# Performance work log

Measured on AMD Instinct MI355X. Metric: run time of the kernel, lower is better.

## Reference

```python
import jax, jax.numpy as jnp
import numpy as np

NUM_HEADS = 32
NUM_KV_HEADS = 8
HEAD_DIM = 64
HIDDEN = 2048
EPS = 1e-05
ROPE_THETA = 1000000.0


def _rmsnorm(x, w):
    # x: [..., head_dim]
    var = jnp.mean(x * x, axis=-1, keepdims=True)
    return w * (x * jax.lax.rsqrt(var + EPS))


def _rope(q, k):
    # q,k: [B, h, T, d]
    T, d = q.shape[2], q.shape[3]
    inv_freq = 1.0 / (ROPE_THETA ** (jnp.arange(0, d, 2, dtype=jnp.float32) / d))
    t = jnp.arange(T, dtype=jnp.float32)
    freqs = jnp.outer(t, inv_freq)               # [T, d/2]
    emb = jnp.concatenate([freqs, freqs], -1)    # [T, d]
    cos = jnp.cos(emb)[None, None].astype(q.dtype)
    sin = jnp.sin(emb)[None, None].astype(q.dtype)

    def rotate(x):
        x1, x2 = x[..., : d // 2], x[..., d // 2 :]
        return jnp.concatenate([-x2, x1], -1)

    return q * cos + rotate(q) * sin, k * cos + rotate(k) * sin


def setup_inputs() -> dict:
    key = jax.random.key(0)
    ks = jax.random.split(key, 7)
    s = 0.02
    x = jax.random.normal(ks[0], (2, 2048, HIDDEN), jnp.float32)
    Wq = jax.random.normal(ks[1], (HIDDEN, NUM_HEADS * HEAD_DIM), jnp.float32) * s
    Wk = jax.random.normal(ks[2], (HIDDEN, NUM_KV_HEADS * HEAD_DIM), jnp.float32) * s
    Wv = jax.random.normal(ks[3], (HIDDEN, NUM_KV_HEADS * HEAD_DIM), jnp.float32) * s
    Wo = jax.random.normal(ks[4], (NUM_HEADS * HEAD_DIM, HIDDEN), jnp.float32) * s
    q_ln_w = jnp.ones((HEAD_DIM,), jnp.float32)
    k_ln_w = jnp.ones((HEAD_DIM,), jnp.float32)
    return {"x": x, "Wq": Wq, "Wk": Wk, "Wv": Wv, "Wo": Wo, "q_ln_w": q_ln_w, "k_ln_w": k_ln_w}


def reference(x, Wq, Wk, Wv, Wo, q_ln_w, k_ln_w):
    B, T, _ = x.shape
    g = NUM_HEADS // NUM_KV_HEADS  # GQA groups = 4
    q = (x @ Wq).reshape(B, T, NUM_HEADS, HEAD_DIM)
    k = (x @ Wk).reshape(B, T, NUM_KV_HEADS, HEAD_DIM)
    v = (x @ Wv).reshape(B, T, NUM_KV_HEADS, HEAD_DIM)
    q = _rmsnorm(q, q_ln_w)
    k = _rmsnorm(k, k_ln_w)
    q = q.transpose(0, 2, 1, 3)  # [B, nh, T, d]
    k = k.transpose(0, 2, 1, 3)  # [B, nkv, T, d]
    v = v.transpose(0, 2, 1, 3)
    q, k = _rope(q, k)
    # native GQA: fold query heads into (kv_head, group) without repeating K/V
    qg = q.reshape(B, NUM_KV_HEADS, g, T, HEAD_DIM)
    scale = 1.0 / jnp.sqrt(jnp.array(HEAD_DIM, q.dtype))
    scores = jnp.einsum("bkgtd,bksd->bkgts", qg, k) * scale  # [B,nkv,g,T,T]
    causal = jnp.tril(jnp.ones((T, T), bool))
    scores = jnp.where(causal, scores, jnp.finfo(scores.dtype).min)
    probs = jax.nn.softmax(scores, axis=-1)
    out = jnp.einsum("bkgts,bksd->bkgtd", probs, v)  # [B,nkv,g,T,d]
    out = out.reshape(B, NUM_HEADS, T, HEAD_DIM).transpose(0, 2, 1, 3).reshape(B, T, -1)
    return out @ Wo
```

## Files before the change

### kernel.cpp

```cpp
#include <hip/hip_runtime.h>
#include <cstdint>
#include <cstddef>

typedef unsigned short u16;
typedef __attribute__((ext_vector_type(8))) short short8;
typedef __attribute__((ext_vector_type(4))) short short4v;
typedef __attribute__((ext_vector_type(4))) float float4v;
typedef __attribute__((ext_vector_type(4))) unsigned short ushort4v;
typedef __attribute__((ext_vector_type(2))) float float2v;

__device__ __forceinline__ u16 f2bf(float f) {
    union { float f; uint32_t u; } x; x.f = f;
    uint32_t r = x.u + 0x7fffu + ((x.u >> 16) & 1u);
    return (u16)(r >> 16);
}
__device__ __forceinline__ uint32_t pack_bf16x2(float lo, float hi) {
    union { float f; uint32_t u; } a, b; a.f = lo; b.f = hi;
    return __builtin_amdgcn_perm(b.u + 0x8000u, a.u + 0x8000u, 0x07060302u);
}

__global__ __launch_bounds__(256) void prep(const float4v* __restrict__ x,
                                            const float* __restrict__ Wq,
                                            const float* __restrict__ Wk,
                                            const float* __restrict__ Wv,
                                            const float* __restrict__ Wo,
                                            ushort4v* __restrict__ xb,
                                            u16* __restrict__ wqkv_t,
                                            u16* __restrict__ wo_t,
                                            float2v* __restrict__ tab) {
    __shared__ float lds[32][33];
    const int bid = blockIdx.x;
    const int tid = threadIdx.x;
    if (bid < 8192) {
        const int i = bid * 256 + tid;
        float4v v = x[i];
        ushort4v o;
        #pragma unroll
        for (int j = 0; j < 4; ++j) o[j] = f2bf(v[j]);
        xb[i] = o;
        return;
    }
    if (bid < 8448) {
        const int idx = (bid - 8192) * 256 + tid;
        const int t = idx >> 5;
        const int i = idx & 31;
        const float invf = exp2f(-(float)i * (19.931568569324174f / 32.0f));
        float sv, cv;
        sincosf((float)t * invf, &sv, &cv);
        float2v o; o[0] = cv; o[1] = sv;
        tab[idx] = o;
        return;
    }
    const float* src;
    int Ns, n0, k0, scol0;
    u16* dst;
    if (bid < 14592) {
        const int id = bid - 8448;
        const int bx = id % 96, by = id / 96;
        n0 = bx * 32; k0 = by * 32;
        if (n0 < 2048)      { src = Wq; Ns = 2048; scol0 = n0; }
        else if (n0 < 2560) { src = Wk; Ns = 512;  scol0 = n0 - 2048; }
        else                { src = Wv; Ns = 512;  scol0 = n0 - 2560; }
        dst = wqkv_t;
    } else {
        const int id = bid - 14592;
        const int bx = id & 63, by = id >> 6;
        n0 = bx * 32; k0 = by * 32;
        src = Wo; Ns = 2048; scol0 = n0;
        dst = wo_t;
    }
    const int row = tid >> 3;
    const int c4  = (tid & 7) * 4;
    const float4v v = *(const float4v*)(src + (size_t)(k0 + row) * Ns + scol0 + c4);
    #pragma unroll
    for (int i = 0; i < 4; ++i) lds[row][c4 + i] = v[i];
    __syncthreads();
    const int nrow = tid >> 3;
    const int k4   = (tid & 7) * 4;
    ushort4v o;
    #pragma unroll
    for (int i = 0; i < 4; ++i) o[i] = f2bf(lds[k4 + i][nrow]);
    *(ushort4v*)(dst + (size_t)(n0 + nrow) * 2048 + k0 + k4) = o;
}

__global__ __launch_bounds__(256, 3) void gemm_bt(const u16* __restrict__ A,
                                                  const u16* __restrict__ Bt,
                                                  float* __restrict__ C,
                                                  int M, int N, int K) {
    __shared__ u16 lds_a[2][128 * 32];
    __shared__ u16 lds_b[2][128 * 32];
    const int tid  = threadIdx.x;
    const int wave = tid >> 6;
    const int lane = tid & 63;
    const int quad = lane >> 4;
    const int l15  = lane & 15;
    const long m0 = (long)blockIdx.x * 128;
    const long n0 = (long)blockIdx.y * 128;
    const int wm = (wave >> 1) * 64;
    const int wn = (wave & 1) * 64;
    const int s_row = tid >> 2;
    const int s_col = (tid & 3) * 8;

    float4v acc[4][4];
    #pragma unroll
    for (int i = 0; i < 4; ++i)
        #pragma unroll
        for (int j = 0; j < 4; ++j)
            #pragma unroll
            for (int r = 0; r < 4; ++r) acc[i][j][r] = 0.0f;

    short8 areg[2], breg[2];
    #pragma unroll
    for (int c = 0; c < 2; ++c) {
        areg[c] = *(const short8*)(A  + (m0 + c * 64 + s_row) * (long)K + s_col);
        breg[c] = *(const short8*)(Bt + (n0 + c * 64 + s_row) * (long)K + s_col);
    }
    #pragma unroll
    for (int c = 0; c < 2; ++c) {
        *(short8*)(lds_a[0] + (c * 64 + s_row) * 32 + s_col) = areg[c];
        *(short8*)(lds_b[0] + (c * 64 + s_row) * 32 + s_col) = breg[c];
    }
    __syncthreads();

    const int n_k = K >> 5;
    for (int it = 0; it < n_k; ++it) {
        const int p = it & 1;
        if (it + 1 < n_k) {
            const int kn = (it + 1) << 5;
            #pragma unroll
            for (int c = 0; c < 2; ++c) {
                areg[c] = *(const short8*)(A  + (m0 + c * 64 + s_row) * (long)K + kn + s_col);
                breg[c] = *(const short8*)(Bt + (n0 + c * 64 + s_row) * (long)K + kn + s_col);
            }
        }
        short8 af[4], bfr[4];
        #pragma unroll
        for (int mt = 0; mt < 4; ++mt)
            af[mt] = *(const short8*)(lds_a[p] + (wm + mt * 16 + l15) * 32 + quad * 8);
        #pragma unroll
        for (int nt = 0; nt < 4; ++nt)
            bfr[nt] = *(const short8*)(lds_b[p] + (wn + nt * 16 + l15) * 32 + quad * 8);
        #pragma unroll
        for (int mt = 0; mt < 4; ++mt)
            #pragma unroll
            for (int nt = 0; nt < 4; ++nt)
                acc[mt][nt] = __builtin_amdgcn_mfma_f32_16x16x32_bf16(af[mt], bfr[nt], acc[mt][nt], 0, 0, 0);
        if (it + 1 < n_k) {
            #pragma unroll
            for (int c = 0; c < 2; ++c) {
                *(short8*)(lds_a[1 - p] + (c * 64 + s_row) * 32 + s_col) = areg[c];
                *(short8*)(lds_b[1 - p] + (c * 64 + s_row) * 32 + s_col) = breg[c];
            }
        }
        __syncthreads();
    }
    #pragma unroll
    for (int mt = 0; mt < 4; ++mt) {
        #pragma unroll
        for (int nt = 0; nt < 4; ++nt) {
            const long gr = m0 + wm + mt * 16 + quad * 4;
            const long gc = n0 + wn + nt * 16 + l15;
            #pragma unroll
            for (int r = 0; r < 4; ++r)
                C[(gr + r) * N + gc] = acc[mt][nt][r];
        }
    }
}

__global__ __launch_bounds__(256, 3) void gemm_qkv(const u16* __restrict__ A,
                                                   const u16* __restrict__ Bt,
                                                   const float* __restrict__ qw,
                                                   const float* __restrict__ kw,
                                                   const float2v* __restrict__ tab,
                                                   u16* __restrict__ Qr,
                                                   u16* __restrict__ Kr,
                                                   u16* __restrict__ Vt) {
    const int K = 2048;
    __shared__ u16 lds_a[2][128 * 32];
    __shared__ u16 lds_b[2][128 * 32];
    const int tid  = threadIdx.x;
    const int wave = tid >> 6;
    const int lane = tid & 63;
    const int quad = lane >> 4;
    const int l15  = lane & 15;
    const long m0 = (long)blockIdx.x * 128;
    const long n0 = (long)blockIdx.y * 128;
    const int wm = (wave >> 1) * 64;
    const int wn = (wave & 1) * 64;
    const int s_row = tid >> 2;
    const int s_col = (tid & 3) * 8;

    float4v acc[4][4];
    #pragma unroll
    for (int i = 0; i < 4; ++i)
        #pragma unroll
        for (int j = 0; j < 4; ++j)
            #pragma unroll
            for (int r = 0; r < 4; ++r) acc[i][j][r] = 0.0f;

    short8 areg[2], breg[2];
    #pragma unroll
    for (int c = 0; c < 2; ++c) {
        areg[c] = *(const short8*)(A  + (m0 + c * 64 + s_row) * (long)K + s_col);
        breg[c] = *(const short8*)(Bt + (n0 + c * 64 + s_row) * (long)K + s_col);
    }
    #pragma unroll
    for (int c = 0; c < 2; ++c) {
        *(short8*)(lds_a[0] + (c * 64 + s_row) * 32 + s_col) = areg[c];
        *(short8*)(lds_b[0] + (c * 64 + s_row) * 32 + s_col) = breg[c];
    }
    __syncthreads();

    const int n_k = K >> 5;
    for (int it = 0; it < n_k; ++it) {
        const int p = it & 1;
        if (it + 1 < n_k) {
            const int kn = (it + 1) << 5;
            #pragma unroll
            for (int c = 0; c < 2; ++c) {
                areg[c] = *(const short8*)(A  + (m0 + c * 64 + s_row) * (long)K + kn + s_col);
                breg[c] = *(const short8*)(Bt + (n0 + c * 64 + s_row) * (long)K + kn + s_col);
            }
        }
        short8 af[4], bfr[4];
        #pragma unroll
        for (int mt = 0; mt < 4; ++mt)
            af[mt] = *(const short8*)(lds_a[p] + (wm + mt * 16 + l15) * 32 + quad * 8);
        #pragma unroll
        for (int nt = 0; nt < 4; ++nt)
            bfr[nt] = *(const short8*)(lds_b[p] + (wn + nt * 16 + l15) * 32 + quad * 8);
        #pragma unroll
        for (int mt = 0; mt < 4; ++mt)
            #pragma unroll
            for (int nt = 0; nt < 4; ++nt)
                acc[mt][nt] = __builtin_amdgcn_mfma_f32_16x16x32_bf16(af[mt], bfr[nt], acc[mt][nt], 0, 0, 0);
        if (it + 1 < n_k) {
            #pragma unroll
            for (int c = 0; c < 2; ++c) {
                *(short8*)(lds_a[1 - p] + (c * 64 + s_row) * 32 + s_col) = areg[c];
                *(short8*)(lds_b[1 - p] + (c * 64 + s_row) * 32 + s_col) = breg[c];
            }
        }
        __syncthreads();
    }

    const int col0 = (int)n0 + wn;
    if (col0 < 2560) {
        const bool isQ = (col0 < 2048);
        const float* lw = isQ ? qw : kw;
        float wreg[4];
        #pragma unroll
        for (int nt = 0; nt < 4; ++nt) wreg[nt] = lw[nt * 16 + l15];
        const float qs = isQ ? 0.18033688011112042f : 1.0f;
        u16* dst = isQ ? (Qr + ((size_t)(col0 >> 6)) * 2048 * 64)
                       : (Kr + ((size_t)((col0 - 2048) >> 6)) * 2048 * 64);
        const size_t head_stride = isQ ? ((size_t)32 * 2048 * 64) : ((size_t)8 * 2048 * 64);
        #pragma unroll
        for (int mt = 0; mt < 4; ++mt) {
            const int gr0 = (int)m0 + wm + mt * 16 + quad * 4;
            const int b = gr0 >> 11, tt0 = gr0 & 2047;
            float rms[4];
            #pragma unroll
            for (int r = 0; r < 4; ++r) {
                float s = 0.0f;
                #pragma unroll
                for (int nt = 0; nt < 4; ++nt) s += acc[mt][nt][r] * acc[mt][nt][r];
                s += __shfl_xor(s, 1);
                s += __shfl_xor(s, 2);
                s += __shfl_xor(s, 4);
                s += __shfl_xor(s, 8);
                rms[r] = rsqrtf(s * (1.0f / 64.0f) + 1e-5f);
            }
            u16* rowp = dst + (size_t)b * head_stride + (size_t)tt0 * 64;
            #pragma unroll
            for (int nt = 0; nt < 2; ++nt) {
                const int i = nt * 16 + l15;
                #pragma unroll
                for (int r = 0; r < 4; ++r) {
                    const float2v cs = tab[(tt0 + r) * 32 + i];
                    const float v1 = acc[mt][nt][r]     * rms[r] * wreg[nt];
                    const float v2 = acc[mt][nt + 2][r] * rms[r] * wreg[nt + 2];
                    const float o1 = (v1 * cs[0] - v2 * cs[1]) * qs;
                    const float o2 = (v2 * cs[0] + v1 * cs[1]) * qs;
                    rowp[(size_t)r * 64 + i]      = f2bf(o1);
                    rowp[(size_t)r * 64 + i + 32] = f2bf(o2);
                }
            }
        }
    } else {
        const int kh = (col0 - 2560) >> 6;
        #pragma unroll
        for (int mt = 0; mt < 4; ++mt) {
            const int gr0 = (int)m0 + wm + mt * 16 + quad * 4;
            const int b = gr0 >> 11, tt0 = gr0 & 2047;
            #pragma unroll
            for (int nt = 0; nt < 4; ++nt) {
                const int d = nt * 16 + l15;
                ushort4v o;
                #pragma unroll
                for (int r = 0; r < 4; ++r) o[r] = f2bf(acc[mt][nt][r]);
                *(ushort4v*)(Vt + (((size_t)(b * 8 + kh)) * 64 + d) * 2048 + tt0) = o;
            }
        }
    }
}

#define KSTR 72
#define VSTR 136
__global__ __launch_bounds__(512, 4) void attn_fwd(const u16* __restrict__ Qr,
                                                   const u16* __restrict__ Kr,
                                                   const u16* __restrict__ Vt,
                                                   u16* __restrict__ Ob) {
    __shared__ u16 lds_k[2][128 * KSTR];
    __shared__ u16 lds_vt[2][64 * VSTR];
    const int tid  = threadIdx.x;
    const int wave = tid >> 6;
    const int lane = tid & 63;
    const int quad = lane >> 4;
    const int l15  = lane & 15;
    const int qxB = blockIdx.x;
    const int qxA = 15 - qxB;
    const int bh = blockIdx.y;
    const int b = bh >> 5, h = bh & 31;
    const int kh = h >> 2;
    const u16* Qh = Qr + ((size_t)(b * 32 + h))  * 2048 * 64;
    const u16* Kh = Kr + ((size_t)(b * 8 + kh))  * 2048 * 64;
    const u16* Vh = Vt + ((size_t)(b * 8 + kh))  * 64 * 2048;

    const int k_key0 = tid >> 3;
    const int k_d0   = (tid & 7) * 8;
    const int v_d0   = tid >> 4;
    const int v_k8   = (tid & 15) * 8;

    const int qrowA = qxA * 128 + wave * 16 + l15;
    const int qrowB = qxB * 128 + wave * 16 + l15;
    short8 qfA[2], qfB[2];
    #pragma unroll
    for (int ks = 0; ks < 2; ++ks) {
        qfA[ks] = *(const short8*)(Qh + (size_t)qrowA * 64 + ks * 32 + quad * 8);
        qfB[ks] = *(const short8*)(Qh + (size_t)qrowB * 64 + ks * 32 + quad * 8);
    }
    short8 qf0 = qfA[0], qf1 = qfA[1];
    int qrow_cur = qrowA;

    float m_i = -3e38f, l_i = 0.0f;
    float4v Oacc[4];
    #pragma unroll
    for (int dt = 0; dt < 4; ++dt)
        #pragma unroll
        for (int r = 0; r < 4; ++r) Oacc[dt][r] = 0.0f;

    short8 kreg[2], vreg[2];
    #pragma unroll
    for (int i = 0; i < 2; ++i) {
        kreg[i] = *(const short8*)(Kh + (size_t)(k_key0 + i * 64) * 64 + k_d0);
        vreg[i] = *(const short8*)(Vh + (size_t)(v_d0 + i * 32) * 2048 + v_k8);
    }
    #pragma unroll
    for (int i = 0; i < 2; ++i) {
        *(short8*)(lds_k[0]  + (k_key0 + i * 64) * KSTR + k_d0) = kreg[i];
        *(short8*)(lds_vt[0] + (v_d0 + i * 32) * VSTR + v_k8)   = vreg[i];
    }
    __syncthreads();

    const int n_it = 17;
    for (int i = 0; i < n_it; ++i) {
        const int p = i & 1;
        const bool last = (i == n_it - 1);
        const int kt_cur = (i <= qxA) ? i : (i - qxA - 1);
        const int kt0 = kt_cur << 7;

        if (!last) {
            const int ip1 = i + 1;
            const int ktn = (ip1 <= qxA) ? ip1 : (ip1 - qxA - 1);
            const size_t nk0 = (size_t)(ktn << 7);
            #pragma unroll
            for (int j = 0; j < 2; ++j) {
                kreg[j] = *(const short8*)(Kh + (nk0 + k_key0 + j * 64) * 64 + k_d0);
                vreg[j] = *(const short8*)(Vh + (size_t)(v_d0 + j * 32) * 2048 + nk0 + v_k8);
            }
        }

        float4v S[8];
        #pragma unroll
        for (int nt = 0; nt < 8; ++nt)
            #pragma unroll
            for (int r = 0; r < 4; ++r) S[nt][r] = 0.0f;
        #pragma unroll
        for (int ks = 0; ks < 2; ++ks) {
            const short8 qf = ks ? qf1 : qf0;
            #pragma unroll
            for (int nt = 0; nt < 8; ++nt) {
                short8 kf = *(const short8*)(lds_k[p] + (nt * 16 + l15) * KSTR + ks * 32 + quad * 8);
                S[nt] = __builtin_amdgcn_mfma_f32_16x16x32_bf16(kf, qf, S[nt], 0, 0, 0);
            }
        }
        if (i == qxA || last) {
            #pragma unroll
            for (int nt = 0; nt < 8; ++nt) {
                const int keyb = kt0 + nt * 16 + quad * 4;
                #pragma unroll
                for (int r = 0; r < 4; ++r)
                    if (keyb + r > qrow_cur) S[nt][r] = -3e38f;
            }
        }
        float mx = S[0][0];
        #pragma unroll
        for (int nt = 0; nt < 8; ++nt)
            #pragma unroll
            for (int r = 0; r < 4; ++r) mx = fmaxf(mx, S[nt][r]);
        mx = fmaxf(mx, __shfl_xor(mx, 16));
        mx = fmaxf(mx, __shfl_xor(mx, 32));
        const float mnew = fmaxf(m_i, mx);
        const float alpha = __builtin_amdgcn_exp2f(m_i - mnew);
        m_i = mnew;
        float rs = 0.0f;
        #pragma unroll
        for (int nt = 0; nt < 8; ++nt)
            #pragma unroll
            for (int r = 0; r < 4; ++r) {
                const float pv = __builtin_amdgcn_exp2f(S[nt][r] - mnew);
                S[nt][r] = pv;
                rs += pv;
            }
        rs += __shfl_xor(rs, 16);
        rs += __shfl_xor(rs, 32);
        l_i = l_i * alpha + rs;
        #pragma unroll
        for (int dt = 0; dt < 4; ++dt)
            #pragma unroll
            for (int r = 0; r < 4; ++r) Oacc[dt][r] *= alpha;

        #pragma unroll
        for (int nt = 0; nt < 8; ++nt) {
            union { uint32_t u[2]; short4v s; } pu;
            pu.u[0] = pack_bf16x2(S[nt][0], S[nt][1]);
            pu.u[1] = pack_bf16x2(S[nt][2], S[nt][3]);
            const short4v pf = pu.s;
            #pragma unroll
            for (int dt = 0; dt < 4; ++dt) {
                const short4v vf = *(const short4v*)(lds_vt[p] + (dt * 16 + l15) * VSTR + nt * 16 + quad * 4);
                Oacc[dt] = __builtin_amdgcn_mfma_f32_16x16x16bf16_1k(vf, pf, Oacc[dt], 0, 0, 0);
            }
        }

        if (i == qxA) {
            const float rl = 1.0f / l_i;
            #pragma unroll
            for (int dt = 0; dt < 4; ++dt) {
                ushort4v o;
                #pragma unroll
                for (int r = 0; r < 4; ++r) o[r] = f2bf(Oacc[dt][r] * rl);
                *(ushort4v*)(Ob + ((size_t)(b * 2048 + qrowA)) * 2048 + h * 64 + dt * 16 + quad * 4) = o;
            }
            m_i = -3e38f;
            l_i = 0.0f;
            qf0 = qfB[0];
            qf1 = qfB[1];
            qrow_cur = qrowB;
        }

        if (!last) {
            #pragma unroll
            for (int j = 0; j < 2; ++j) {
                *(short8*)(lds_k[1 - p]  + (k_key0 + j * 64) * KSTR + k_d0) = kreg[j];
                *(short8*)(lds_vt[1 - p] + (v_d0 + j * 32) * VSTR + v_k8)   = vreg[j];
            }
        }
        __syncthreads();
    }
    const float rl = 1.0f / l_i;
    #pragma unroll
    for (int dt = 0; dt < 4; ++dt) {
        ushort4v o;
        #pragma unroll
        for (int r = 0; r < 4; ++r) o[r] = f2bf(Oacc[dt][r] * rl);
        *(ushort4v*)(Ob + ((size_t)(b * 2048 + qrowB)) * 2048 + h * 64 + dt * 16 + quad * 4) = o;
    }
}

extern "C" void kernel_launch(void* const* d_in, const int* in_sizes, int n_in,
                              void* d_out, int out_size, void* d_ws, size_t ws_size,
                              hipStream_t stream) {
    (void)in_sizes; (void)n_in; (void)out_size; (void)ws_size;
    const float* x  = (const float*)d_in[0];
    const float* Wq = (const float*)d_in[1];
    const float* Wk = (const float*)d_in[2];
    const float* Wv = (const float*)d_in[3];
    const float* Wo = (const float*)d_in[4];
    const float* qw = (const float*)d_in[5];
    const float* kw = (const float*)d_in[6];
    float* out = (float*)d_out;

    char* ws = (char*)d_ws;
    size_t off = 0;
    auto alloc = [&](size_t bytes) {
        char* p = ws + off;
        off += (bytes + 255) & ~(size_t)255;
        return p;
    };
    u16* xb     = (u16*)alloc((size_t)8388608 * 2);
    u16* wqkv_t = (u16*)alloc((size_t)3072 * 2048 * 2);
    u16* wo_t   = (u16*)alloc((size_t)2048 * 2048 * 2);
    u16* q_r    = (u16*)alloc((size_t)2 * 32 * 2048 * 64 * 2);
    u16* k_r    = (u16*)alloc((size_t)2 * 8 * 2048 * 64 * 2);
    u16* v_r    = (u16*)alloc((size_t)2 * 8 * 64 * 2048 * 2);
    float2v* rtab = (float2v*)alloc((size_t)2048 * 32 * 8);
    u16* attnb  = xb;

    hipLaunchKernelGGL(prep, dim3(18688), dim3(256), 0, stream,
                       (const float4v*)x, Wq, Wk, Wv, Wo,
                       (ushort4v*)xb, wqkv_t, wo_t, rtab);
    hipLaunchKernelGGL(gemm_qkv, dim3(32, 24), dim3(256), 0, stream,
                       xb, wqkv_t, qw, kw, rtab, q_r, k_r, v_r);
    hipLaunchKernelGGL(attn_fwd, dim3(8, 64), dim3(512), 0, stream, q_r, k_r, v_r, attnb);
    hipLaunchKernelGGL(gemm_bt, dim3(32, 16), dim3(256), 0, stream,
                       attnb, wo_t, out, 4096, 2048, 2048);
}
```

Before: 295.5 us.

## Use direct global-to-LDS loads in GEMMs and lazy softmax rescaling in attention

The two GEMM kernels drop the register-staged double-buffered LDS pipeline and instead load tiles straight from global memory into a single LDS buffer using global_load_lds, with a barrier before and after the compute. This removes the VGPR staging and ds_write instructions and halves LDS use, but it no longer overlaps the next tile's global loads with the current MFMAs. In attention, the online-softmax rescale of O and l is skipped unless the row max grows by more than 8 (in log2 units), which saves exp and multiply work per tile. Because that path now skips the alpha multiply, Oacc is explicitly zeroed when a query row finishes.

```diff
diff --git a/kernel.cpp b/kernel.cpp
--- a/kernel.cpp
+++ b/kernel.cpp
@@ -17,6 +17,11 @@
 __device__ __forceinline__ uint32_t pack_bf16x2(float lo, float hi) {
     union { float f; uint32_t u; } a, b; a.f = lo; b.f = hi;
     return __builtin_amdgcn_perm(b.u + 0x8000u, a.u + 0x8000u, 0x07060302u);
+}
+__device__ __forceinline__ void gl_lds16(const u16* g, u16* l) {
+    __builtin_amdgcn_global_load_lds(
+        (const __attribute__((address_space(1))) void*)g,
+        (__attribute__((address_space(3))) void*)l, 16, 0, 0);
 }
 
 __global__ __launch_bounds__(256) void prep(const float4v* __restrict__ x,
@@ -87,8 +92,8 @@
                                                   const u16* __restrict__ Bt,
                                                   float* __restrict__ C,
                                                   int M, int N, int K) {
-    __shared__ u16 lds_a[2][128 * 32];
-    __shared__ u16 lds_b[2][128 * 32];
+    __shared__ u16 lds_a[128 * 32];
+    __shared__ u16 lds_b[128 * 32];
     const int tid  = threadIdx.x;
     const int wave = tid >> 6;
     const int lane = tid & 63;
@@ -109,49 +114,33 @@
             #pragma unroll
             for (int r = 0; r < 4; ++r) acc[i][j][r] = 0.0f;
 
-    short8 areg[2], breg[2];
-    #pragma unroll
-    for (int c = 0; c < 2; ++c) {
-        areg[c] = *(const short8*)(A  + (m0 + c * 64 + s_row) * (long)K + s_col);
-        breg[c] = *(const short8*)(Bt + (n0 + c * 64 + s_row) * (long)K + s_col);
-    }
-    #pragma unroll
-    for (int c = 0; c < 2; ++c) {
-        *(short8*)(lds_a[0] + (c * 64 + s_row) * 32 + s_col) = areg[c];
-        *(short8*)(lds_b[0] + (c * 64 + s_row) * 32 + s_col) = breg[c];
-    }
-    __syncthreads();
+    const u16* ga0 = A  + (m0 + s_row) * (long)K + s_col;
+    const u16* ga1 = ga0 + 64 * (long)K;
+    const u16* gb0 = Bt + (n0 + s_row) * (long)K + s_col;
+    const u16* gb1 = gb0 + 64 * (long)K;
+    u16* la = lds_a + tid * 8;
+    u16* lb = lds_b + tid * 8;
 
     const int n_k = K >> 5;
     for (int it = 0; it < n_k; ++it) {
-        const int p = it & 1;
-        if (it + 1 < n_k) {
-            const int kn = (it + 1) << 5;
-            #pragma unroll
-            for (int c = 0; c < 2; ++c) {
-                areg[c] = *(const short8*)(A  + (m0 + c * 64 + s_row) * (long)K + kn + s_col);
-                breg[c] = *(const short8*)(Bt + (n0 + c * 64 + s_row) * (long)K + kn + s_col);
-            }
-        }
+        const int k0 = it << 5;
+        gl_lds16(ga0 + k0, la);
+        gl_lds16(ga1 + k0, la + 2048);
+        gl_lds16(gb0 + k0, lb);
+        gl_lds16(gb1 + k0, lb + 2048);
+        __syncthreads();
         short8 af[4], bfr[4];
         #pragma unroll
         for (int mt = 0; mt < 4; ++mt)
-            af[mt] = *(const short8*)(lds_a[p] + (wm + mt * 16 + l15) * 32 + quad * 8);
+            af[mt] = *(const short8*)(lds_a + (wm + mt * 16 + l15) * 32 + quad * 8);
         #pragma unroll
         for (int nt = 0; nt < 4; ++nt)
-            bfr[nt] = *(const short8*)(lds_b[p] + (wn + nt * 16 + l15) * 32 + quad * 8);
+            bfr[nt] = *(const short8*)(lds_b + (wn + nt * 16 + l15) * 32 + quad * 8);
         #pragma unroll
         for (int mt = 0; mt < 4; ++mt)
             #pragma unroll
             for (int nt = 0; nt < 4; ++nt)
                 acc[mt][nt] = __builtin_amdgcn_mfma_f32_16x16x32_bf16(af[mt], bfr[nt], acc[mt][nt], 0, 0, 0);
-        if (it + 1 < n_k) {
-            #pragma unroll
-            for (int c = 0; c < 2; ++c) {
-                *(short8*)(lds_a[1 - p] + (c * 64 + s_row) * 32 + s_col) = areg[c];
-                *(short8*)(lds_b[1 - p] + (c * 64 + s_row) * 32 + s_col) = breg[c];
-            }
-        }
         __syncthreads();
     }
     #pragma unroll
@@ -176,8 +165,8 @@
                                                    u16* __restrict__ Kr,
                                                    u16* __restrict__ Vt) {
     const int K = 2048;
-    __shared__ u16 lds_a[2][128 * 32];
-    __shared__ u16 lds_b[2][128 * 32];
+    __shared__ u16 lds_a[128 * 32];
+    __shared__ u16 lds_b[128 * 32];
     const int tid  = threadIdx.x;
     const int wave = tid >> 6;
     const int lane = tid & 63;
@@ -198,49 +187,33 @@
             #pragma unroll
             for (int r = 0; r < 4; ++r) acc[i][j][r] = 0.0f;
 
-    short8 areg[2], breg[2];
-    #pragma unroll
-    for (int c = 0; c < 2; ++c) {
-        areg[c] = *(const short8*)(A  + (m0 + c * 64 + s_row) * (long)K + s_col);
-        breg[c] = *(const short8*)(Bt + (n0 + c * 64 + s_row) * (long)K + s_col);
-    }
-    #pragma unroll
-    for (int c = 0; c < 2; ++c) {
-        *(short8*)(lds_a[0] + (c * 64 + s_row) * 32 + s_col) = areg[c];
-        *(short8*)(lds_b[0] + (c * 64 + s_row) * 32 + s_col) = breg[c];
-    }
-    __syncthreads();
+    const u16* ga0 = A  + (m0 + s_row) * (long)K + s_col;
+    const u16* ga1 = ga0 + 64 * (long)K;
+    const u16* gb0 = Bt + (n0 + s_row) * (long)K + s_col;
+    const u16* gb1 = gb0 + 64 * (long)K;
+    u16* la = lds_a + tid * 8;
+    u16* lb = lds_b + tid * 8;
 
     const int n_k = K >> 5;
     for (int it = 0; it < n_k; ++it) {
-        const int p = it & 1;
-        if (it + 1 < n_k) {
-            const int kn = (it + 1) << 5;
-            #pragma unroll
-            for (int c = 0; c < 2; ++c) {
-                areg[c] = *(const short8*)(A  + (m0 + c * 64 + s_row) * (long)K + kn + s_col);
-                breg[c] = *(const short8*)(Bt + (n0 + c * 64 + s_row) * (long)K + kn + s_col);
-            }
-        }
+        const int k0 = it << 5;
+        gl_lds16(ga0 + k0, la);
+        gl_lds16(ga1 + k0, la + 2048);
+        gl_lds16(gb0 + k0, lb);
+        gl_lds16(gb1 + k0, lb + 2048);
+        __syncthreads();
         short8 af[4], bfr[4];
         #pragma unroll
         for (int mt = 0; mt < 4; ++mt)
-            af[mt] = *(const short8*)(lds_a[p] + (wm + mt * 16 + l15) * 32 + quad * 8);
+            af[mt] = *(const short8*)(lds_a + (wm + mt * 16 + l15) * 32 + quad * 8);
         #pragma unroll
         for (int nt = 0; nt < 4; ++nt)
-            bfr[nt] = *(const short8*)(lds_b[p] + (wn + nt * 16 + l15) * 32 + quad * 8);
+            bfr[nt] = *(const short8*)(lds_b + (wn + nt * 16 + l15) * 32 + quad * 8);
         #pragma unroll
         for (int mt = 0; mt < 4; ++mt)
             #pragma unroll
             for (int nt = 0; nt < 4; ++nt)
                 acc[mt][nt] = __builtin_amdgcn_mfma_f32_16x16x32_bf16(af[mt], bfr[nt], acc[mt][nt], 0, 0, 0);
-        if (it + 1 < n_k) {
-            #pragma unroll
-            for (int c = 0; c < 2; ++c) {
-                *(short8*)(lds_a[1 - p] + (c * 64 + s_row) * 32 + s_col) = areg[c];
-                *(short8*)(lds_b[1 - p] + (c * 64 + s_row) * 32 + s_col) = breg[c];
-            }
-        }
         __syncthreads();
     }
 
@@ -411,25 +384,28 @@
             for (int r = 0; r < 4; ++r) mx = fmaxf(mx, S[nt][r]);
         mx = fmaxf(mx, __shfl_xor(mx, 16));
         mx = fmaxf(mx, __shfl_xor(mx, 32));
-        const float mnew = fmaxf(m_i, mx);
-        const float alpha = __builtin_amdgcn_exp2f(m_i - mnew);
-        m_i = mnew;
+        if (!__all(mx <= m_i + 8.0f)) {
+            const float mnew = fmaxf(m_i, mx);
+            const float alpha = __builtin_amdgcn_exp2f(m_i - mnew);
+            m_i = mnew;
+            l_i *= alpha;
+            #pragma unroll
+            for (int dt = 0; dt < 4; ++dt)
+                #pragma unroll
+                for (int r = 0; r < 4; ++r) Oacc[dt][r] *= alpha;
+        }
         float rs = 0.0f;
         #pragma unroll
         for (int nt = 0; nt < 8; ++nt)
             #pragma unroll
             for (int r = 0; r < 4; ++r) {
-                const float pv = __builtin_amdgcn_exp2f(S[nt][r] - mnew);
+                const float pv = __builtin_amdgcn_exp2f(S[nt][r] - m_i);
                 S[nt][r] = pv;
                 rs += pv;
             }
         rs += __shfl_xor(rs, 16);
         rs += __shfl_xor(rs, 32);
-        l_i = l_i * alpha + rs;
-        #pragma unroll
-        for (int dt = 0; dt < 4; ++dt)
-            #pragma unroll
-            for (int r = 0; r < 4; ++r) Oacc[dt][r] *= alpha;
+        l_i += rs;
 
         #pragma unroll
         for (int nt = 0; nt < 8; ++nt) {
@@ -455,6 +431,10 @@
             }
             m_i = -3e38f;
             l_i = 0.0f;
+            #pragma unroll
+            for (int dt = 0; dt < 4; ++dt)
+                #pragma unroll
+                for (int r = 0; r < 4; ++r) Oacc[dt][r] = 0.0f;
             qf0 = qfB[0];
             qf1 = qfB[1];
             qrow_cur = qrowB;
```

New measurement: 294.7 us. No clear change (-0.3%).
